# Optimization experiments

Measured on AMD Instinct MI355X. Metric: run time of the kernel, lower is better.

Reference implementation:

```python
import jax, jax.numpy as jnp
import numpy as np

DIM = 512
NUM_HEADS = 8
NUM_BLOCKS = 16
# NOTE: original code computes head_dim from FULL dim (before the reduce layer),
# so scale = (dim // num_heads) ** -0.5 = 64 ** -0.5, even though the actual
# per-head dim after reduce is 32. We preserve this quirk faithfully.
SCALE = (DIM // NUM_HEADS) ** -0.5


def setup_inputs() -> dict:
    key = jax.random.key(0)
    ks = jax.random.split(key, 5)
    B, N = 4, 4096
    C = DIM // 2
    x = jax.random.normal(ks[0], (B, N, DIM), dtype=jnp.float32)
    reduce_w = jax.random.normal(ks[1], (DIM, C), dtype=jnp.float32) * (DIM ** -0.5)
    qkv_w = jax.random.normal(ks[2], (C, 3 * C), dtype=jnp.float32) * (C ** -0.5)
    proj_w = jax.random.normal(ks[3], (C, DIM), dtype=jnp.float32) * (C ** -0.5)
    proj_b = jnp.zeros((DIM,), dtype=jnp.float32)
    return {"x": x, "reduce_w": reduce_w, "qkv_w": qkv_w,
            "proj_w": proj_w, "proj_b": proj_b}


def reference(x, reduce_w, qkv_w, proj_w, proj_b):
    B, N, _ = x.shape
    xr = x @ reduce_w                      # [B, N, C]  (C = dim/2)
    C = xr.shape[-1]
    H = NUM_HEADS
    d = C // H
    qkv = (xr @ qkv_w).reshape(B, N, 3, H, d).transpose(2, 0, 3, 1, 4)  # [3,B,H,N,d]
    q, k, v = qkv[0], qkv[1], qkv[2]
    bs = N // NUM_BLOCKS                   # block (chunk) size
    # block-diagonal local attention: reshape seq into independent blocks
    qb = q.reshape(B, H, NUM_BLOCKS, bs, d)
    kb = k.reshape(B, H, NUM_BLOCKS, bs, d)
    vb = v.reshape(B, H, NUM_BLOCKS, bs, d)
    attn = jnp.einsum('bhnqd,bhnkd->bhnqk', qb, kb) * SCALE
    attn = jax.nn.softmax(attn, axis=-1)
    ob = jnp.einsum('bhnqk,bhnkd->bhnqd', attn, vb)   # [B,H,Nb,bs,d]
    # torch: per-block transpose(1,2) then cat on dim=1 -> [B, N, H, d]
    o = ob.transpose(0, 2, 3, 1, 4).reshape(B, N, C)
    return o @ proj_w + proj_b
```

## Files before the change

### kernel.cpp

```cpp
#include <hip/hip_runtime.h>
#include <hip/hip_fp16.h>

typedef _Float16 half_t;
typedef _Float16 f16x8 __attribute__((ext_vector_type(8)));
typedef __fp16 fp16x2 __attribute__((ext_vector_type(2)));
typedef float f32x4 __attribute__((ext_vector_type(4)));

#define MFMA_F16(a, b, c) __builtin_amdgcn_mfma_f32_16x16x32_f16((a), (b), (c), 0, 0, 0)

static __device__ inline unsigned pkrtz(float a, float b) {
    union { fp16x2 h; unsigned u; } c;
    c.h = __builtin_amdgcn_cvt_pkrtz(a, b);
    return c.u;
}

__device__ __forceinline__ void gload16(const half_t* g, half_t* l) {
    __builtin_amdgcn_global_load_lds(
        (const __attribute__((address_space(1))) void*)g,
        (__attribute__((address_space(3))) void*)l, 16, 0, 0);
}

__global__ __launch_bounds__(256) void prep(
    const float* __restrict__ x, const float* __restrict__ qw,
    const float* __restrict__ rw, const float* __restrict__ pw,
    half_t* __restrict__ x_h, half_t* __restrict__ pw_t, half_t* __restrict__ Wt) {
    __shared__ __align__(16) char smem[24576];
    const int bid = blockIdx.x, tid = threadIdx.x;

    if (bid < 48) {
        char* As = smem;
        char* Bs = smem + 8192;
        const int M0 = (bid % 12) * 64, N0 = (bid / 12) * 128;
        const int lane = tid & 63, w = tid >> 6;
        const int l15 = lane & 15, l4 = lane >> 4;
        const int wrow = (w >> 1) * 32, wcol = (w & 1) * 64;
        const int pa = (l15 & 7) << 4;

        f32x4 acc[2][4];
#pragma unroll
        for (int i = 0; i < 2; ++i)
#pragma unroll
            for (int j = 0; j < 4; ++j) acc[i][j] = (f32x4){0.f, 0.f, 0.f, 0.f};

        for (int kc = 0; kc < 4; ++kc) {
            int c0 = kc * 64;
            __syncthreads();
#pragma unroll
            for (int i = 0; i < 2; ++i) {
                int j = tid + i * 256;
                int row = j >> 3, e8 = (j & 7) * 8;
                float s = (M0 + row) < 256 ? 0.125f : 1.f;
                f16x8 v;
#pragma unroll
                for (int e = 0; e < 8; ++e)
                    v[e] = (half_t)(qw[(size_t)(c0 + e8 + e) * 768 + M0 + row] * s);
                *(f16x8*)(As + row * 128 + ((e8 * 2) ^ ((row & 7) << 4))) = v;
            }
#pragma unroll
            for (int i = 0; i < 4; ++i) {
                int j = tid + i * 256;
                int row = j >> 3, e8 = (j & 7) * 8;
                const float* p = rw + (size_t)(N0 + row) * 256 + c0 + e8;
                float4 u0 = *(const float4*)p;
                float4 u1 = *(const float4*)(p + 4);
                f16x8 v;
                v[0] = (half_t)u0.x; v[1] = (half_t)u0.y;
                v[2] = (half_t)u0.z; v[3] = (half_t)u0.w;
                v[4] = (half_t)u1.x; v[5] = (half_t)u1.y;
                v[6] = (half_t)u1.z; v[7] = (half_t)u1.w;
                *(f16x8*)(Bs + row * 128 + ((e8 * 2) ^ ((row & 7) << 4))) = v;
            }
            __syncthreads();
#pragma unroll
            for (int ki = 0; ki < 2; ++ki) {
                f16x8 af[2], bf[4];
#pragma unroll
                for (int mi = 0; mi < 2; ++mi) {
                    int row = wrow + mi * 16 + l15;
                    af[mi] = *(const f16x8*)(As + row * 128 + (((ki * 4 + l4) << 4) ^ pa));
                }
#pragma unroll
                for (int nj = 0; nj < 4; ++nj) {
                    int row = wcol + nj * 16 + l15;
                    bf[nj] = *(const f16x8*)(Bs + row * 128 + (((ki * 4 + l4) << 4) ^ pa));
                }
#pragma unroll
                for (int mi = 0; mi < 2; ++mi)
#pragma unroll
                    for (int nj = 0; nj < 4; ++nj)
                        acc[mi][nj] = MFMA_F16(af[mi], bf[nj], acc[mi][nj]);
            }
        }
#pragma unroll
        for (int mi = 0; mi < 2; ++mi)
#pragma unroll
            for (int nj = 0; nj < 4; ++nj)
#pragma unroll
                for (int reg = 0; reg < 4; ++reg) {
                    int grow = M0 + wrow + mi * 16 + l4 * 4 + reg;
                    int gcol = N0 + wcol + nj * 16 + l15;
                    Wt[(size_t)grow * 512 + gcol] = (half_t)acc[mi][nj][reg];
                }
        return;
    }

    if (bid < 80) {
        half_t* tile = (half_t*)smem;
        int t = bid - 48;
        int R0 = (t >> 3) * 64, C0 = (t & 7) * 64;
#pragma unroll
        for (int e = 0; e < 16; ++e) {
            int idx = tid + e * 256;
            int r = idx >> 6, c = idx & 63;
            tile[r * 72 + c] = (half_t)pw[(size_t)(R0 + r) * 512 + C0 + c];
        }
        __syncthreads();
#pragma unroll
        for (int e = 0; e < 16; ++e) {
            int idx = tid + e * 256;
            int c = idx >> 6, r = idx & 63;
            pw_t[(size_t)(C0 + c) * 256 + R0 + r] = tile[r * 72 + c];
        }
        return;
    }

    int i8 = ((bid - 80) * 256 + tid) * 8;
    float4 a = *(const float4*)(x + i8);
    float4 b = *(const float4*)(x + i8 + 4);
    f16x8 v;
    v[0] = (half_t)a.x; v[1] = (half_t)a.y; v[2] = (half_t)a.z; v[3] = (half_t)a.w;
    v[4] = (half_t)b.x; v[5] = (half_t)b.y; v[6] = (half_t)b.z; v[7] = (half_t)b.w;
    *(f16x8*)(x_h + i8) = v;
}

template <int EPI, int K, int NB>
__global__ __launch_bounds__(256) void gemm_f16(
    const half_t* __restrict__ A, const half_t* __restrict__ Bt,
    void* __restrict__ Dst, const float* __restrict__ bias) {
    constexpr int nkt = K >> 6;
    constexpr int NLB = NB / 32;
    constexpr int NJ = NB / 32;
    constexpr int BUFSZ = 16384 + NB * 128;
    __shared__ __align__(16) char smem[2 * BUFSZ];

    const int tid = threadIdx.x;
    const int lane = tid & 63, w = tid >> 6;
    const int l15 = lane & 15, l4 = lane >> 4;
    const int wrow = (w >> 1) * 64, wcol = (w & 1) * (NB / 2);
    const int bm0 = blockIdx.x * 128;
    const int bn0 = blockIdx.y * NB;

    const half_t* srcA[4];
#pragma unroll
    for (int i = 0; i < 4; ++i) {
        int J = w * 256 + i * 64 + lane;
        int row = J >> 3, c = (J & 7) ^ (row & 7);
        srcA[i] = A + (size_t)(bm0 + row) * K + c * 8;
    }
    const half_t* srcB[NLB];
#pragma unroll
    for (int i = 0; i < NLB; ++i) {
        int J = w * (64 * NLB) + i * 64 + lane;
        int row = J >> 3, c = (J & 7) ^ (row & 7);
        srcB[i] = Bt + (size_t)(bn0 + row) * K + c * 8;
    }

    auto STAGE = [&](int kt) {
        char* As = smem + (kt & 1) * BUFSZ;
        char* Bs = As + 16384;
#pragma unroll
        for (int i = 0; i < 4; ++i)
            gload16(srcA[i] + kt * 64, (half_t*)(As + (w * 4 + i) * 1024));
#pragma unroll
        for (int i = 0; i < NLB; ++i)
            gload16(srcB[i] + kt * 64, (half_t*)(Bs + (w * NLB + i) * 1024));
    };

    f32x4 acc[4][NJ];
#pragma unroll
    for (int i = 0; i < 4; ++i)
#pragma unroll
        for (int j = 0; j < NJ; ++j) acc[i][j] = (f32x4){0.f, 0.f, 0.f, 0.f};

    const int pa = (l15 & 7) << 4;

    STAGE(0);
#pragma unroll
    for (int kt = 0; kt < nkt; ++kt) {
        if (kt + 1 < nkt) {
            STAGE(kt + 1);
            asm volatile("s_waitcnt vmcnt(%0)" ::"i"(4 + NLB) : "memory");
        } else {
            asm volatile("s_waitcnt vmcnt(0)" ::: "memory");
        }
        __builtin_amdgcn_s_barrier();
        __builtin_amdgcn_sched_barrier(0);

        const char* As = smem + (kt & 1) * BUFSZ;
        const char* Bs = As + 16384;
#pragma unroll
        for (int ki = 0; ki < 2; ++ki) {
            f16x8 af[4], bf[NJ];
#pragma unroll
            for (int mi = 0; mi < 4; ++mi) {
                int row = wrow + mi * 16 + l15;
                af[mi] = *(const f16x8*)(As + row * 128 + (((ki * 4 + l4) << 4) ^ pa));
            }
#pragma unroll
            for (int nj = 0; nj < NJ; ++nj) {
                int row = wcol + nj * 16 + l15;
                bf[nj] = *(const f16x8*)(Bs + row * 128 + (((ki * 4 + l4) << 4) ^ pa));
            }
#pragma unroll
            for (int mi = 0; mi < 4; ++mi)
#pragma unroll
                for (int nj = 0; nj < NJ; ++nj)
                    acc[mi][nj] = MFMA_F16(af[mi], bf[nj], acc[mi][nj]);
        }
        __builtin_amdgcn_sched_barrier(0);
        __builtin_amdgcn_s_barrier();
    }

#pragma unroll
    for (int mi = 0; mi < 4; ++mi) {
#pragma unroll
        for (int nj = 0; nj < NJ; ++nj) {
#pragma unroll
            for (int reg = 0; reg < 4; ++reg) {
                int grow = bm0 + wrow + mi * 16 + l4 * 4 + reg;
                int gcol = bn0 + wcol + nj * 16 + l15;
                float val = acc[mi][nj][reg];
                if (EPI == 1) {
                    int t = gcol >> 8, h = (gcol >> 5) & 7, dd = gcol & 31;
                    int b = grow >> 12, n = grow & 4095;
                    int blk = n >> 8, r = n & 255;
                    size_t base = (size_t)t * 4194304 +
                                  (size_t)((((b << 3) + h) << 4) + blk) * 8192;
                    size_t idx = (t == 2) ? base + (size_t)dd * 256 + r
                                          : base + (size_t)r * 32 + dd;
                    ((half_t*)Dst)[idx] = (half_t)val;
                } else {
                    ((float*)Dst)[(size_t)grow * 512 + gcol] = val + bias[gcol];
                }
            }
        }
    }
}

__global__ __launch_bounds__(256, 4) void attn_f16(const half_t* __restrict__ qkv_ws,
                                                   half_t* __restrict__ o_ws) {
    const int bid = blockIdx.x;
    const int blkid = ((bid >> 4) << 3) | (bid & 7);
    const int hh = (bid >> 3) & 1;
    const int b = blkid >> 7, h = (blkid >> 4) & 7, blk = blkid & 15;
    const half_t* Q  = qkv_ws + (size_t)blkid * 8192;
    const half_t* Kp = qkv_ws + 4194304 + (size_t)blkid * 8192;
    const half_t* VT = qkv_ws + 8388608 + (size_t)blkid * 8192;

    const int tid = threadIdx.x, lane = tid & 63, w = tid >> 6;
    const int l15 = lane & 15, l4 = lane >> 4;
    const int qb = hh * 128 + w * 32;

    f16x8 aq[2];
    aq[0] = *(const f16x8*)(Q + (qb + l15) * 32 + l4 * 8);
    aq[1] = *(const f16x8*)(Q + (qb + 16 + l15) * 32 + l4 * 8);

    float m_run[2] = {-1e30f, -1e30f}, s_run[2] = {0.f, 0.f};
    f32x4 acc_o[2][2];
#pragma unroll
    for (int qg = 0; qg < 2; ++qg)
#pragma unroll
        for (int fo = 0; fo < 2; ++fo) acc_o[qg][fo] = (f32x4){0.f, 0.f, 0.f, 0.f};
    const f32x4 zero4 = (f32x4){0.f, 0.f, 0.f, 0.f};

    for (int kt = 0; kt < 4; ++kt) {
        f16x8 ka[4];
#pragma unroll
        for (int t = 0; t < 4; ++t)
            ka[t] = *(const f16x8*)(Kp + (kt * 64 + t * 16 + l15) * 32 + l4 * 8);
        f16x8 bv[2][2];
#pragma unroll
        for (int c = 0; c < 2; ++c)
#pragma unroll
            for (int fo = 0; fo < 2; ++fo)
                bv[c][fo] = *(const f16x8*)(VT + (fo * 16 + l15) * 256 + kt * 64 + c * 32 + l4 * 8);

#pragma unroll
        for (int qg = 0; qg < 2; ++qg) {
            f32x4 st[4];
#pragma unroll
            for (int t = 0; t < 4; ++t) st[t] = MFMA_F16(ka[t], aq[qg], zero4);

            float mt = -1e30f;
#pragma unroll
            for (int t = 0; t < 4; ++t)
#pragma unroll
                for (int r = 0; r < 4; ++r) mt = fmaxf(mt, st[t][r]);
            mt = fmaxf(mt, __shfl_xor(mt, 16));
            mt = fmaxf(mt, __shfl_xor(mt, 32));

            float mn = fmaxf(m_run[qg], mt);
            float corr = __expf(m_run[qg] - mn);
            m_run[qg] = mn;

            float p[4][4];
            float ps = 0.f;
#pragma unroll
            for (int t = 0; t < 4; ++t)
#pragma unroll
                for (int r = 0; r < 4; ++r) {
                    float e = __expf(st[t][r] - mn);
                    p[t][r] = e;
                    ps += e;
                }
            ps += __shfl_xor(ps, 16);
            ps += __shfl_xor(ps, 32);
            s_run[qg] = s_run[qg] * corr + ps;

            float corrs[4];
#pragma unroll
            for (int r = 0; r < 4; ++r) corrs[r] = __shfl(corr, (l4 << 2) | r);
#pragma unroll
            for (int fo = 0; fo < 2; ++fo)
#pragma unroll
                for (int r = 0; r < 4; ++r) acc_o[qg][fo][r] *= corrs[r];

#pragma unroll
            for (int c = 0; c < 2; ++c) {
                unsigned pk0[2], pk1[2];
#pragma unroll
                for (int rp = 0; rp < 2; ++rp) {
                    pk0[rp] = pkrtz(p[2 * c][2 * rp], p[2 * c][2 * rp + 1]);
                    pk1[rp] = pkrtz(p[2 * c + 1][2 * rp], p[2 * c + 1][2 * rp + 1]);
                }
                union { unsigned u[4]; f16x8 v; } au;
#pragma unroll
                for (int j = 0; j < 4; ++j) {
                    int src = l15 + ((((l4 & 1) << 1) + (j >> 1)) << 4);
                    unsigned g0 = (unsigned)__shfl((int)pk0[j & 1], src);
                    unsigned g1 = (unsigned)__shfl((int)pk1[j & 1], src);
                    au.u[j] = (l4 < 2) ? g0 : g1;
                }
#pragma unroll
                for (int fo = 0; fo < 2; ++fo)
                    acc_o[qg][fo] = MFMA_F16(au.v, bv[c][fo], acc_o[qg][fo]);
            }
        }
    }

#pragma unroll
    for (int qg = 0; qg < 2; ++qg) {
        float inv = 1.f / s_run[qg];
        float sinv[4];
#pragma unroll
        for (int r = 0; r < 4; ++r) sinv[r] = __shfl(inv, (l4 << 2) | r);
#pragma unroll
        for (int fo = 0; fo < 2; ++fo)
#pragma unroll
            for (int r = 0; r < 4; ++r) {
                int grow = b * 4096 + blk * 256 + qb + qg * 16 + l4 * 4 + r;
                o_ws[(size_t)grow * 256 + h * 32 + fo * 16 + l15] =
                    (half_t)(acc_o[qg][fo][r] * sinv[r]);
            }
    }
}

extern "C" void kernel_launch(void* const* d_in, const int* in_sizes, int n_in,
                              void* d_out, int out_size, void* d_ws, size_t ws_size,
                              hipStream_t stream) {
    const float* x        = (const float*)d_in[0];
    const float* reduce_w = (const float*)d_in[1];
    const float* qkv_w    = (const float*)d_in[2];
    const float* proj_w   = (const float*)d_in[3];
    const float* proj_b   = (const float*)d_in[4];
    char* ws = (char*)d_ws;

    half_t* qkv_ws = (half_t*)ws;
    half_t* o_buf  = (half_t*)(ws + 25165824);
    half_t* pw_t   = (half_t*)(ws + 33554432);
    half_t* Wt     = (half_t*)(ws + 33816576);
    half_t* x_h    = (half_t*)(ws + 34603008);

    prep<<<4176, 256, 0, stream>>>(x, qkv_w, reduce_w, proj_w, x_h, pw_t, Wt);
    gemm_f16<1, 512, 192><<<dim3(128, 4), 256, 0, stream>>>(x_h, Wt, qkv_ws, nullptr);
    attn_f16<<<1024, 256, 0, stream>>>(qkv_ws, o_buf);
    gemm_f16<2, 256, 128><<<dim3(128, 4), 256, 0, stream>>>(o_buf, pw_t, d_out, proj_b);
}
```

Before: 71.46 us.

## Fuse fp32-to-fp16 conversion of x into the QKV GEMM A-operand load

Removes the separate pass that converted x to fp16 in the prep kernel. The QKV GEMM now reads fp32 x directly into registers, converts it with pkrtz, and feeds it straight into the MFMAs without going through LDS, while B is still staged through LDS. This avoids writing and re-reading the fp16 copy of x. In exchange, each of the 4 column blocks re-reads the fp32 rows at twice the bytes. The A loads are also plain register loads that are not coalesced across the tile, and each iteration waits with vmcnt(0), which gives less overlap.

```diff
diff --git a/kernel.cpp b/kernel.cpp
--- a/kernel.cpp
+++ b/kernel.cpp
@@ -21,9 +21,9 @@
 }
 
 __global__ __launch_bounds__(256) void prep(
-    const float* __restrict__ x, const float* __restrict__ qw,
-    const float* __restrict__ rw, const float* __restrict__ pw,
-    half_t* __restrict__ x_h, half_t* __restrict__ pw_t, half_t* __restrict__ Wt) {
+    const float* __restrict__ qw, const float* __restrict__ rw,
+    const float* __restrict__ pw, half_t* __restrict__ pw_t,
+    half_t* __restrict__ Wt) {
     __shared__ __align__(16) char smem[24576];
     const int bid = blockIdx.x, tid = threadIdx.x;
 
@@ -104,43 +104,33 @@
         return;
     }
 
-    if (bid < 80) {
-        half_t* tile = (half_t*)smem;
-        int t = bid - 48;
-        int R0 = (t >> 3) * 64, C0 = (t & 7) * 64;
-#pragma unroll
-        for (int e = 0; e < 16; ++e) {
-            int idx = tid + e * 256;
-            int r = idx >> 6, c = idx & 63;
-            tile[r * 72 + c] = (half_t)pw[(size_t)(R0 + r) * 512 + C0 + c];
-        }
-        __syncthreads();
-#pragma unroll
-        for (int e = 0; e < 16; ++e) {
-            int idx = tid + e * 256;
-            int c = idx >> 6, r = idx & 63;
-            pw_t[(size_t)(C0 + c) * 256 + R0 + r] = tile[r * 72 + c];
-        }
-        return;
-    }
-
-    int i8 = ((bid - 80) * 256 + tid) * 8;
-    float4 a = *(const float4*)(x + i8);
-    float4 b = *(const float4*)(x + i8 + 4);
-    f16x8 v;
-    v[0] = (half_t)a.x; v[1] = (half_t)a.y; v[2] = (half_t)a.z; v[3] = (half_t)a.w;
-    v[4] = (half_t)b.x; v[5] = (half_t)b.y; v[6] = (half_t)b.z; v[7] = (half_t)b.w;
-    *(f16x8*)(x_h + i8) = v;
-}
-
-template <int EPI, int K, int NB>
+    half_t* tile = (half_t*)smem;
+    int t = bid - 48;
+    int R0 = (t >> 3) * 64, C0 = (t & 7) * 64;
+#pragma unroll
+    for (int e = 0; e < 16; ++e) {
+        int idx = tid + e * 256;
+        int r = idx >> 6, c = idx & 63;
+        tile[r * 72 + c] = (half_t)pw[(size_t)(R0 + r) * 512 + C0 + c];
+    }
+    __syncthreads();
+#pragma unroll
+    for (int e = 0; e < 16; ++e) {
+        int idx = tid + e * 256;
+        int c = idx >> 6, r = idx & 63;
+        pw_t[(size_t)(C0 + c) * 256 + R0 + r] = tile[r * 72 + c];
+    }
+}
+
+template <int EPI, int K, int NB, bool AF32>
 __global__ __launch_bounds__(256) void gemm_f16(
-    const half_t* __restrict__ A, const half_t* __restrict__ Bt,
+    const void* __restrict__ Aop, const half_t* __restrict__ Bt,
     void* __restrict__ Dst, const float* __restrict__ bias) {
     constexpr int nkt = K >> 6;
     constexpr int NLB = NB / 32;
     constexpr int NJ = NB / 32;
-    constexpr int BUFSZ = 16384 + NB * 128;
+    constexpr int ABYTES = AF32 ? 0 : 16384;
+    constexpr int BUFSZ = ABYTES + NB * 128;
     __shared__ __align__(16) char smem[2 * BUFSZ];
 
     const int tid = threadIdx.x;
@@ -150,13 +140,6 @@
     const int bm0 = blockIdx.x * 128;
     const int bn0 = blockIdx.y * NB;
 
-    const half_t* srcA[4];
-#pragma unroll
-    for (int i = 0; i < 4; ++i) {
-        int J = w * 256 + i * 64 + lane;
-        int row = J >> 3, c = (J & 7) ^ (row & 7);
-        srcA[i] = A + (size_t)(bm0 + row) * K + c * 8;
-    }
     const half_t* srcB[NLB];
 #pragma unroll
     for (int i = 0; i < NLB; ++i) {
@@ -164,13 +147,8 @@
         int row = J >> 3, c = (J & 7) ^ (row & 7);
         srcB[i] = Bt + (size_t)(bn0 + row) * K + c * 8;
     }
-
-    auto STAGE = [&](int kt) {
-        char* As = smem + (kt & 1) * BUFSZ;
-        char* Bs = As + 16384;
-#pragma unroll
-        for (int i = 0; i < 4; ++i)
-            gload16(srcA[i] + kt * 64, (half_t*)(As + (w * 4 + i) * 1024));
+    auto STAGE_B = [&](int kt) {
+        char* Bs = smem + (kt & 1) * BUFSZ + ABYTES;
 #pragma unroll
         for (int i = 0; i < NLB; ++i)
             gload16(srcB[i] + kt * 64, (half_t*)(Bs + (w * NLB + i) * 1024));
@@ -184,41 +162,121 @@
 
     const int pa = (l15 & 7) << 4;
 
-    STAGE(0);
-#pragma unroll
-    for (int kt = 0; kt < nkt; ++kt) {
-        if (kt + 1 < nkt) {
-            STAGE(kt + 1);
-            asm volatile("s_waitcnt vmcnt(%0)" ::"i"(4 + NLB) : "memory");
-        } else {
+    if (AF32) {
+        const float* Af = (const float*)Aop;
+        const float* aptr[4];
+#pragma unroll
+        for (int mi = 0; mi < 4; ++mi)
+            aptr[mi] = Af + (size_t)(bm0 + wrow + mi * 16 + l15) * K + l4 * 8;
+
+        float4 araw[4][2][2];
+        f16x8 aq16[4][2];
+        auto LOADA = [&](int kt) {
+#pragma unroll
+            for (int mi = 0; mi < 4; ++mi)
+#pragma unroll
+                for (int ki = 0; ki < 2; ++ki) {
+                    araw[mi][ki][0] = *(const float4*)(aptr[mi] + kt * 64 + ki * 32);
+                    araw[mi][ki][1] = *(const float4*)(aptr[mi] + kt * 64 + ki * 32 + 4);
+                }
+        };
+        auto CVT = [&]() {
+#pragma unroll
+            for (int mi = 0; mi < 4; ++mi)
+#pragma unroll
+                for (int ki = 0; ki < 2; ++ki) {
+                    union { unsigned u[4]; f16x8 v; } cu;
+                    cu.u[0] = pkrtz(araw[mi][ki][0].x, araw[mi][ki][0].y);
+                    cu.u[1] = pkrtz(araw[mi][ki][0].z, araw[mi][ki][0].w);
+                    cu.u[2] = pkrtz(araw[mi][ki][1].x, araw[mi][ki][1].y);
+                    cu.u[3] = pkrtz(araw[mi][ki][1].z, araw[mi][ki][1].w);
+                    aq16[mi][ki] = cu.v;
+                }
+        };
+
+        LOADA(0);
+        STAGE_B(0);
+        CVT();
+#pragma unroll
+        for (int kt = 0; kt < nkt; ++kt) {
             asm volatile("s_waitcnt vmcnt(0)" ::: "memory");
-        }
-        __builtin_amdgcn_s_barrier();
-        __builtin_amdgcn_sched_barrier(0);
-
-        const char* As = smem + (kt & 1) * BUFSZ;
-        const char* Bs = As + 16384;
-#pragma unroll
-        for (int ki = 0; ki < 2; ++ki) {
-            f16x8 af[4], bf[NJ];
-#pragma unroll
-            for (int mi = 0; mi < 4; ++mi) {
-                int row = wrow + mi * 16 + l15;
-                af[mi] = *(const f16x8*)(As + row * 128 + (((ki * 4 + l4) << 4) ^ pa));
-            }
-#pragma unroll
-            for (int nj = 0; nj < NJ; ++nj) {
-                int row = wcol + nj * 16 + l15;
-                bf[nj] = *(const f16x8*)(Bs + row * 128 + (((ki * 4 + l4) << 4) ^ pa));
-            }
-#pragma unroll
-            for (int mi = 0; mi < 4; ++mi)
-#pragma unroll
-                for (int nj = 0; nj < NJ; ++nj)
-                    acc[mi][nj] = MFMA_F16(af[mi], bf[nj], acc[mi][nj]);
-        }
-        __builtin_amdgcn_sched_barrier(0);
-        __builtin_amdgcn_s_barrier();
+            __builtin_amdgcn_s_barrier();
+            if (kt + 1 < nkt) {
+                STAGE_B(kt + 1);
+                LOADA(kt + 1);
+            }
+            __builtin_amdgcn_sched_barrier(0);
+            const char* Bs = smem + (kt & 1) * BUFSZ;
+#pragma unroll
+            for (int ki = 0; ki < 2; ++ki) {
+                f16x8 bf[NJ];
+#pragma unroll
+                for (int nj = 0; nj < NJ; ++nj) {
+                    int row = wcol + nj * 16 + l15;
+                    bf[nj] = *(const f16x8*)(Bs + row * 128 + (((ki * 4 + l4) << 4) ^ pa));
+                }
+#pragma unroll
+                for (int mi = 0; mi < 4; ++mi)
+#pragma unroll
+                    for (int nj = 0; nj < NJ; ++nj)
+                        acc[mi][nj] = MFMA_F16(aq16[mi][ki], bf[nj], acc[mi][nj]);
+            }
+            if (kt + 1 < nkt) CVT();
+        }
+    } else {
+        const half_t* A = (const half_t*)Aop;
+        const half_t* srcA[4];
+#pragma unroll
+        for (int i = 0; i < 4; ++i) {
+            int J = w * 256 + i * 64 + lane;
+            int row = J >> 3, c = (J & 7) ^ (row & 7);
+            srcA[i] = A + (size_t)(bm0 + row) * K + c * 8;
+        }
+        auto STAGE_A = [&](int kt) {
+            char* As = smem + (kt & 1) * BUFSZ;
+#pragma unroll
+            for (int i = 0; i < 4; ++i)
+                gload16(srcA[i] + kt * 64, (half_t*)(As + (w * 4 + i) * 1024));
+        };
+
+        STAGE_A(0);
+        STAGE_B(0);
+#pragma unroll
+        for (int kt = 0; kt < nkt; ++kt) {
+            if (kt + 1 < nkt) {
+                STAGE_A(kt + 1);
+                STAGE_B(kt + 1);
+                asm volatile("s_waitcnt vmcnt(%0)" ::"i"(4 + NLB) : "memory");
+            } else {
+                asm volatile("s_waitcnt vmcnt(0)" ::: "memory");
+            }
+            __builtin_amdgcn_s_barrier();
+            __builtin_amdgcn_sched_barrier(0);
+
+            const char* As = smem + (kt & 1) * BUFSZ;
+            const char* Bs = As + 16384;
+#pragma unroll
+            for (int ki = 0; ki < 2; ++ki) {
+                f16x8 af[4], bf[NJ];
+#pragma unroll
+                for (int mi = 0; mi < 4; ++mi) {
+                    int row = wrow + mi * 16 + l15;
+                    af[mi] = *(const f16x8*)(As + row * 128 + (((ki * 4 + l4) << 4) ^ pa));
+                }
+#pragma unroll
+                for (int nj = 0; nj < NJ; ++nj) {
+                    int row = wcol + nj * 16 + l15;
+                    bf[nj] = *(const f16x8*)(Bs + row * 128 + (((ki * 4 + l4) << 4) ^ pa));
+                }
+#pragma unroll
+                for (int mi = 0; mi < 4; ++mi)
+#pragma unroll
+                    for (int nj = 0; nj < NJ; ++nj)
+                        acc[mi][nj] = MFMA_F16(af[mi], bf[nj], acc[mi][nj]);
+            }
+            __builtin_amdgcn_sched_barrier(0);
+            __builtin_amdgcn_s_barrier();
+        }
     }
 
 #pragma unroll
@@ -379,10 +437,9 @@
     half_t* o_buf  = (half_t*)(ws + 25165824);
     half_t* pw_t   = (half_t*)(ws + 33554432);
     half_t* Wt     = (half_t*)(ws + 33816576);
-    half_t* x_h    = (half_t*)(ws + 34603008);
-
-    prep<<<4176, 256, 0, stream>>>(x, qkv_w, reduce_w, proj_w, x_h, pw_t, Wt);
-    gemm_f16<1, 512, 192><<<dim3(128, 4), 256, 0, stream>>>(x_h, Wt, qkv_ws, nullptr);
+
+    prep<<<80, 256, 0, stream>>>(qkv_w, reduce_w, proj_w, pw_t, Wt);
+    gemm_f16<1, 512, 192, true><<<dim3(128, 4), 256, 0, stream>>>(x, Wt, qkv_ws, nullptr);
     attn_f16<<<1024, 256, 0, stream>>>(qkv_ws, o_buf);
-    gemm_f16<2, 256, 128><<<dim3(128, 4), 256, 0, stream>>>(o_buf, pw_t, d_out, proj_b);
-}
+    gemm_f16<2, 256, 128, false><<<dim3(128, 4), 256, 0, stream>>>(o_buf, pw_t, d_out, proj_b);
+}
```

New measurement: 98.89 us. 38.4% more time.
